# Performance work log

Hardware: AMD Instinct MI355X
Metric: run time of the kernel (lower is better)

Reference implementation:

```python
import jax, jax.numpy as jnp
import numpy as np

B, U, D, N, O = 128, 16, 256, 1024, 256
RES_CONN, IN_CONN, BIAS_P = 0.2, 0.2, 0.5


def _fixed_bernoulli(rng, heads, rows, cols, conn):
    # each column has exactly nb = int(conn*rows) ones (as in the torch code)
    nb = max(1, int(conn * rows))
    r = rng.random((heads, rows, cols))
    thr = np.sort(r, axis=1)[:, nb - 1:nb, :]
    return (r <= thr).astype(np.float32)


def setup_inputs() -> dict:
    rng = np.random.default_rng(0)
    # recurrent weights: normal * fixed-bernoulli mask, normalized by spectral radius
    W = rng.normal(size=(U, N, N)).astype(np.float32) * _fixed_bernoulli(rng, U, N, N, RES_CONN)
    sr0 = np.abs(np.linalg.eigvals(W.astype(np.float64))).max(axis=-1).astype(np.float32).reshape(U, 1, 1)
    W = W / sr0
    Win = _fixed_bernoulli(rng, U, D, N, IN_CONN)
    bias = (rng.random((U, 1, N)) < BIAS_P).astype(np.float32)
    Wout = rng.normal(size=(U, N, O)).astype(np.float32)
    adaptive_lr = rng.random((U, D, 1)).astype(np.float32)
    sr = rng.random((U, 1, 1)).astype(np.float32)
    temperature = np.ones((1,), np.float32)
    X = rng.normal(size=(B, U, D)).astype(np.float32)
    state = rng.normal(size=(B, U, N)).astype(np.float32)
    arrs = dict(X=X, state=state, W=W, Win=Win, bias=bias, Wout=Wout,
                sr=sr, adaptive_lr=adaptive_lr, temperature=temperature)
    return {k: jnp.asarray(v) for k, v in arrs.items()}


def reference(X, state, W, Win, bias, Wout, sr, adaptive_lr, temperature):
    # X: [B,U,D] -> [B,U,1,D]; state: [B,U,N] -> [B,U,1,N]
    x = X[:, :, None, :]
    s = state[:, :, None, :]
    # adaptive per-unit learning rate: softmax over the units axis
    lr = jax.nn.softmax(jnp.einsum('buid,udk->buik', x, adaptive_lr) / temperature, axis=1)  # [B,U,1,1]
    feed = jnp.einsum('buid,udn->buin', x, Win)            # [B,U,1,N]
    echo = jnp.einsum('buin,unm->buim', s, W * sr) + bias  # [B,U,1,N]
    new_state = (1.0 - lr) * s + lr * jnp.tanh(feed + echo)
    output = jnp.einsum('buin,uno->buio', new_state, Wout)  # [B,U,1,O]
    return new_state[:, :, 0, :], output[:, :, 0, :]
```

## Files before the change

kernel.cpp:

```cpp
#include <hip/hip_runtime.h>
#include <math.h>

#define Bsz 128
#define Usz 16
#define Dsz 256
#define Nsz 1024
#define Osz 256

typedef __attribute__((ext_vector_type(4))) float f32x4;
typedef __attribute__((ext_vector_type(8))) short bf16x8;
typedef __attribute__((ext_vector_type(4))) unsigned int u32x4;

union cell_u { u32x4 u; bf16x8 b; };

__device__ __forceinline__ unsigned int fbits(float f) {
    union { float f; unsigned int u; } v; v.f = f; return v.u;
}
__device__ __forceinline__ unsigned int pk(float lo, float hi) {
    return __builtin_amdgcn_perm(fbits(hi), fbits(lo), 0x07060302u);
}
__device__ __forceinline__ bf16x8 pk8s(const float* x, float s) {
    float t[8];
    #pragma unroll
    for (int i = 0; i < 8; i++) t[i] = x[i] * s;
    cell_u r;
    r.u[0] = pk(t[0], t[1]); r.u[1] = pk(t[2], t[3]);
    r.u[2] = pk(t[4], t[5]); r.u[3] = pk(t[6], t[7]);
    return r.b;
}

__global__ __launch_bounds__(256)
void lr_kernel(const float* __restrict__ X, const float* __restrict__ alr,
               const float* __restrict__ temp, float* __restrict__ lr)
{
    const int b = blockIdx.x;
    const int t = threadIdx.x;
    const int u = t >> 4;
    const int l = t & 15;
    const float* xp = X + ((size_t)b * Usz + u) * Dsz;
    const float* ap = alr + (size_t)u * Dsz;
    float s = 0.f;
    for (int d = l; d < Dsz; d += 16) s += xp[d] * ap[d];
    s += __shfl_down(s, 8, 16);
    s += __shfl_down(s, 4, 16);
    s += __shfl_down(s, 2, 16);
    s += __shfl_down(s, 1, 16);
    __shared__ float logits[16];
    if (l == 0) logits[u] = s;
    __syncthreads();
    if (t < 16) {
        const float T = temp[0];
        float m = -1e30f;
        #pragma unroll
        for (int i = 0; i < 16; i++) m = fmaxf(m, logits[i] / T);
        float sum = 0.f;
        #pragma unroll
        for (int i = 0; i < 16; i++) sum += expf(logits[i] / T - m);
        lr[(size_t)b * Usz + t] = expf(logits[t] / T - m) / sum;
    }
}

__global__ __launch_bounds__(256)
void state_mfma(const float* __restrict__ X, const float* __restrict__ state,
                const float* __restrict__ W, const float* __restrict__ Win,
                const float* __restrict__ bias, const float* __restrict__ sr,
                const float* __restrict__ lr, float* __restrict__ out0)
{
    const int id = blockIdx.x;
    const int u  = id & 15;
    const int nt = (id >> 4) & 15;
    const int mt = id >> 8;

    const int tid  = threadIdx.x;
    const int wave = tid >> 6, lane = tid & 63;
    const int l16  = lane & 15, kgl = lane >> 4;
    const int wm = wave & 1, wn = wave >> 1;

    const int row0 = mt * 64 + wm * 32 + l16;
    const int col0 = nt * 64 + wn * 32 + l16;

    const float sru = sr[u];

    const float* Ax0 = X + ((size_t)row0 * Usz + u) * Dsz;
    const float* Ax1 = X + ((size_t)(row0 + 16) * Usz + u) * Dsz;
    const float* Ae0 = state + ((size_t)row0 * Usz + u) * Nsz;
    const float* Ae1 = state + ((size_t)(row0 + 16) * Usz + u) * Nsz;
    const float* Bf  = Win + (size_t)u * Dsz * Nsz + col0;
    const float* Be  = W   + (size_t)u * Nsz * Nsz + col0;

    f32x4 acc[2][2] = {};

    auto loadStep = [&](int step, float (&A0)[8], float (&A1)[8],
                        float (&B0)[8], float (&B1)[8]) {
        const int kb = step * 32 + kgl * 8;
        const float *pa0, *pa1, *pb;
        if (kb < Dsz) {
            pa0 = Ax0 + kb; pa1 = Ax1 + kb; pb = Bf + (size_t)kb * Nsz;
        } else {
            const int kk = kb - Dsz;
            pa0 = Ae0 + kk; pa1 = Ae1 + kk; pb = Be + (size_t)kk * Nsz;
        }
        *(f32x4*)&A0[0] = *(const f32x4*)pa0;
        *(f32x4*)&A0[4] = *(const f32x4*)(pa0 + 4);
        *(f32x4*)&A1[0] = *(const f32x4*)pa1;
        *(f32x4*)&A1[4] = *(const f32x4*)(pa1 + 4);
        #pragma unroll
        for (int j = 0; j < 8; j++) {
            B0[j] = pb[(size_t)j * Nsz];
            B1[j] = pb[(size_t)j * Nsz + 16];
        }
    };
    auto compute = [&](int step, float (&A0)[8], float (&A1)[8],
                       float (&B0)[8], float (&B1)[8]) {
        const float asc = (step < 8) ? 1.f : sru;
        const bf16x8 af0 = pk8s(A0, asc), af1 = pk8s(A1, asc);
        const bf16x8 bf0 = pk8s(B0, 1.f), bf1 = pk8s(B1, 1.f);
        acc[0][0] = __builtin_amdgcn_mfma_f32_16x16x32_bf16(af0, bf0, acc[0][0], 0, 0, 0);
        acc[0][1] = __builtin_amdgcn_mfma_f32_16x16x32_bf16(af0, bf1, acc[0][1], 0, 0, 0);
        acc[1][0] = __builtin_amdgcn_mfma_f32_16x16x32_bf16(af1, bf0, acc[1][0], 0, 0, 0);
        acc[1][1] = __builtin_amdgcn_mfma_f32_16x16x32_bf16(af1, bf1, acc[1][1], 0, 0, 0);
    };

    float A0a[8], A1a[8], B0a[8], B1a[8];
    float A0b[8], A1b[8], B0b[8], B1b[8];

    loadStep(0, A0a, A1a, B0a, B1a);
    for (int s = 0; s < 40; s += 2) {
        loadStep(s + 1, A0b, A1b, B0b, B1b);
        compute(s, A0a, A1a, B0a, B1a);
        if (s + 2 < 40) loadStep(s + 2, A0a, A1a, B0a, B1a);
        compute(s + 1, A0b, A1b, B0b, B1b);
    }

    #pragma unroll
    for (int ni = 0; ni < 2; ni++) {
        const int gcol = nt * 64 + wn * 32 + ni * 16 + l16;
        const float bi = bias[u * Nsz + gcol];
        #pragma unroll
        for (int mi = 0; mi < 2; mi++) {
            #pragma unroll
            for (int rg = 0; rg < 4; rg++) {
                const int grow = mt * 64 + wm * 32 + mi * 16 + kgl * 4 + rg;
                const size_t idx = ((size_t)grow * Usz + u) * Nsz + gcol;
                const float th = tanhf(acc[mi][ni][rg] + bi);
                const float sv = state[idx];
                const float lv = lr[grow * Usz + u];
                out0[idx] = (1.f - lv) * sv + lv * th;
            }
        }
    }
}

__global__ __launch_bounds__(256)
void out_mfma(const float* __restrict__ ns, const float* __restrict__ Wout,
              float* __restrict__ out1)
{
    const int w  = blockIdx.x * 4 + (threadIdx.x >> 6);
    const int u  = w & 15;
    const int ot = (w >> 4) & 15;
    const int mtw = w >> 8;

    const int lane = threadIdx.x & 63;
    const int l16  = lane & 15, kgl = lane >> 4;

    const float* Ap = ns + ((size_t)(mtw * 16 + l16) * Usz + u) * Nsz;
    const float* Bp = Wout + (size_t)u * Nsz * Osz + ot * 16 + l16;

    f32x4 acc = {};

    auto loadStep = [&](int step, float (&A)[8], float (&B)[8]) {
        const int kb = step * 32 + kgl * 8;
        *(f32x4*)&A[0] = *(const f32x4*)(Ap + kb);
        *(f32x4*)&A[4] = *(const f32x4*)(Ap + kb + 4);
        const float* bp = Bp + (size_t)kb * Osz;
        #pragma unroll
        for (int j = 0; j < 8; j++) B[j] = bp[(size_t)j * Osz];
    };
    auto compute = [&](float (&A)[8], float (&B)[8]) {
        const bf16x8 af = pk8s(A, 1.f);
        const bf16x8 bf = pk8s(B, 1.f);
        acc = __builtin_amdgcn_mfma_f32_16x16x32_bf16(af, bf, acc, 0, 0, 0);
    };

    float Aa[8], Ba[8], Ab[8], Bb[8];
    loadStep(0, Aa, Ba);
    for (int s = 0; s < 32; s += 2) {
        loadStep(s + 1, Ab, Bb);
        compute(Aa, Ba);
        if (s + 2 < 32) loadStep(s + 2, Aa, Ba);
        compute(Ab, Bb);
    }

    const int gcol = ot * 16 + l16;
    #pragma unroll
    for (int rg = 0; rg < 4; rg++) {
        const int grow = mtw * 16 + kgl * 4 + rg;
        out1[((size_t)grow * Usz + u) * Osz + gcol] = acc[rg];
    }
}

extern "C" void kernel_launch(void* const* d_in, const int* in_sizes, int n_in,
                              void* d_out, int out_size, void* d_ws, size_t ws_size,
                              hipStream_t stream)
{
    (void)in_sizes; (void)n_in; (void)out_size; (void)ws_size;
    const float* X     = (const float*)d_in[0];
    const float* state = (const float*)d_in[1];
    const float* W     = (const float*)d_in[2];
    const float* Win   = (const float*)d_in[3];
    const float* bias  = (const float*)d_in[4];
    const float* Wout  = (const float*)d_in[5];
    const float* sr    = (const float*)d_in[6];
    const float* alr   = (const float*)d_in[7];
    const float* temp  = (const float*)d_in[8];

    float* out0 = (float*)d_out;
    float* out1 = out0 + (size_t)Bsz * Usz * Nsz;
    float* lr   = (float*)d_ws;

    lr_kernel<<<Bsz, 256, 0, stream>>>(X, alr, temp, lr);
    state_mfma<<<512, 256, 0, stream>>>(X, state, W, Win, bias, sr, lr, out0);
    out_mfma<<<512, 256, 0, stream>>>(out0, Wout, out1);
}
```

Measured before the change: 218.2 us.

## Stage A tiles in LDS with full-batch M tiles and split-K output GEMM

```diff
diff --git a/kernel.cpp b/kernel.cpp
--- a/kernel.cpp
+++ b/kernel.cpp
@@ -6,12 +6,15 @@
 #define Dsz 256
 #define Nsz 1024
 #define Osz 256
-
+#define BK  64
+
+typedef __attribute__((ext_vector_type(2))) unsigned int u32x2;
+typedef __attribute__((ext_vector_type(4))) unsigned int u32x4;
 typedef __attribute__((ext_vector_type(4))) float f32x4;
 typedef __attribute__((ext_vector_type(8))) short bf16x8;
-typedef __attribute__((ext_vector_type(4))) unsigned int u32x4;
 
 union cell_u { u32x4 u; bf16x8 b; };
+union cell2_u { u32x2 u; };
 
 __device__ __forceinline__ unsigned int fbits(float f) {
     union { float f; unsigned int u; } v; v.f = f; return v.u;
@@ -19,13 +22,17 @@
 __device__ __forceinline__ unsigned int pk(float lo, float hi) {
     return __builtin_amdgcn_perm(fbits(hi), fbits(lo), 0x07060302u);
 }
-__device__ __forceinline__ bf16x8 pk8s(const float* x, float s) {
-    float t[8];
-    #pragma unroll
-    for (int i = 0; i < 8; i++) t[i] = x[i] * s;
+__device__ __forceinline__ u32x2 pk4(f32x4 v, float s) {
+    v *= s;
+    u32x2 r; r[0] = pk(v[0], v[1]); r[1] = pk(v[2], v[3]);
+    return r;
+}
+__device__ __forceinline__ bf16x8 ldB8(const float* p, size_t str) {
+    const float x0 = p[0],       x1 = p[str],     x2 = p[2*str], x3 = p[3*str];
+    const float x4 = p[4*str],   x5 = p[5*str],   x6 = p[6*str], x7 = p[7*str];
     cell_u r;
-    r.u[0] = pk(t[0], t[1]); r.u[1] = pk(t[2], t[3]);
-    r.u[2] = pk(t[4], t[5]); r.u[3] = pk(t[6], t[7]);
+    r.u[0] = pk(x0, x1); r.u[1] = pk(x2, x3);
+    r.u[2] = pk(x4, x5); r.u[3] = pk(x6, x7);
     return r.b;
 }
 
@@ -61,75 +68,80 @@
 }
 
 __global__ __launch_bounds__(256)
-void state_mfma(const float* __restrict__ X, const float* __restrict__ state,
+void state_gemm(const float* __restrict__ X, const float* __restrict__ state,
                 const float* __restrict__ W, const float* __restrict__ Win,
                 const float* __restrict__ bias, const float* __restrict__ sr,
                 const float* __restrict__ lr, float* __restrict__ out0)
 {
     const int id = blockIdx.x;
     const int u  = id & 15;
-    const int nt = (id >> 4) & 15;
-    const int mt = id >> 8;
+    const int nt = id >> 4;
 
     const int tid  = threadIdx.x;
     const int wave = tid >> 6, lane = tid & 63;
     const int l16  = lane & 15, kgl = lane >> 4;
     const int wm = wave & 1, wn = wave >> 1;
 
-    const int row0 = mt * 64 + wm * 32 + l16;
-    const int col0 = nt * 64 + wn * 32 + l16;
+    __shared__ unsigned short As[2][128 * 72];
 
     const float sru = sr[u];
 
-    const float* Ax0 = X + ((size_t)row0 * Usz + u) * Dsz;
-    const float* Ax1 = X + ((size_t)(row0 + 16) * Usz + u) * Dsz;
-    const float* Ae0 = state + ((size_t)row0 * Usz + u) * Nsz;
-    const float* Ae1 = state + ((size_t)(row0 + 16) * Usz + u) * Nsz;
-    const float* Bf  = Win + (size_t)u * Dsz * Nsz + col0;
-    const float* Be  = W   + (size_t)u * Nsz * Nsz + col0;
-
-    f32x4 acc[2][2] = {};
-
-    auto loadStep = [&](int step, float (&A0)[8], float (&A1)[8],
-                        float (&B0)[8], float (&B1)[8]) {
-        const int kb = step * 32 + kgl * 8;
-        const float *pa0, *pa1, *pb;
-        if (kb < Dsz) {
-            pa0 = Ax0 + kb; pa1 = Ax1 + kb; pb = Bf + (size_t)kb * Nsz;
+    const int r0 = tid >> 4;
+    const int c  = tid & 15;
+
+    f32x4 ra[8];
+
+    auto ldA = [&](int s) {
+        const int k0 = s * BK;
+        if (k0 < Dsz) {
+            const float* base = X + ((size_t)r0 * Usz + u) * Dsz + k0 + c * 4;
+            #pragma unroll
+            for (int i = 0; i < 8; i++)
+                ra[i] = *(const f32x4*)(base + (size_t)16 * i * Usz * Dsz);
         } else {
-            const int kk = kb - Dsz;
-            pa0 = Ae0 + kk; pa1 = Ae1 + kk; pb = Be + (size_t)kk * Nsz;
-        }
-        *(f32x4*)&A0[0] = *(const f32x4*)pa0;
-        *(f32x4*)&A0[4] = *(const f32x4*)(pa0 + 4);
-        *(f32x4*)&A1[0] = *(const f32x4*)pa1;
-        *(f32x4*)&A1[4] = *(const f32x4*)(pa1 + 4);
-        #pragma unroll
-        for (int j = 0; j < 8; j++) {
-            B0[j] = pb[(size_t)j * Nsz];
-            B1[j] = pb[(size_t)j * Nsz + 16];
-        }
-    };
-    auto compute = [&](int step, float (&A0)[8], float (&A1)[8],
-                       float (&B0)[8], float (&B1)[8]) {
-        const float asc = (step < 8) ? 1.f : sru;
-        const bf16x8 af0 = pk8s(A0, asc), af1 = pk8s(A1, asc);
-        const bf16x8 bf0 = pk8s(B0, 1.f), bf1 = pk8s(B1, 1.f);
-        acc[0][0] = __builtin_amdgcn_mfma_f32_16x16x32_bf16(af0, bf0, acc[0][0], 0, 0, 0);
-        acc[0][1] = __builtin_amdgcn_mfma_f32_16x16x32_bf16(af0, bf1, acc[0][1], 0, 0, 0);
-        acc[1][0] = __builtin_amdgcn_mfma_f32_16x16x32_bf16(af1, bf0, acc[1][0], 0, 0, 0);
-        acc[1][1] = __builtin_amdgcn_mfma_f32_16x16x32_bf16(af1, bf1, acc[1][1], 0, 0, 0);
-    };
-
-    float A0a[8], A1a[8], B0a[8], B1a[8];
-    float A0b[8], A1b[8], B0b[8], B1b[8];
-
-    loadStep(0, A0a, A1a, B0a, B1a);
-    for (int s = 0; s < 40; s += 2) {
-        loadStep(s + 1, A0b, A1b, B0b, B1b);
-        compute(s, A0a, A1a, B0a, B1a);
-        if (s + 2 < 40) loadStep(s + 2, A0a, A1a, B0a, B1a);
-        compute(s + 1, A0b, A1b, B0b, B1b);
+            const float* base = state + ((size_t)r0 * Usz + u) * Nsz + (k0 - Dsz) + c * 4;
+            #pragma unroll
+            for (int i = 0; i < 8; i++)
+                ra[i] = *(const f32x4*)(base + (size_t)16 * i * Usz * Nsz);
+        }
+    };
+    auto wrA = [&](int p, float sc) {
+        #pragma unroll
+        for (int i = 0; i < 8; i++)
+            *(u32x2*)&As[p][(r0 + 16 * i) * 72 + c * 4] = pk4(ra[i], sc);
+    };
+
+    f32x4 acc[4][2] = {};
+
+    auto comp = [&](int s, int p) {
+        const int k0 = s * BK;
+        const float* bbase = (k0 < Dsz)
+            ? Win + (size_t)u * Dsz * Nsz + (size_t)k0 * Nsz
+            : W   + (size_t)u * Nsz * Nsz + (size_t)(k0 - Dsz) * Nsz;
+        const int col = nt * 64 + wn * 32 + l16;
+        #pragma unroll
+        for (int kk = 0; kk < 2; kk++) {
+            const float* bp = bbase + (size_t)(kk * 32 + kgl * 8) * Nsz + col;
+            const bf16x8 bf0 = ldB8(bp, Nsz);
+            const bf16x8 bf1 = ldB8(bp + 16, Nsz);
+            #pragma unroll
+            for (int mi = 0; mi < 4; mi++) {
+                const bf16x8 af = *(const bf16x8*)&As[p][(wm * 64 + mi * 16 + l16) * 72 + kk * 32 + kgl * 8];
+                acc[mi][0] = __builtin_amdgcn_mfma_f32_16x16x32_bf16(af, bf0, acc[mi][0], 0, 0, 0);
+                acc[mi][1] = __builtin_amdgcn_mfma_f32_16x16x32_bf16(af, bf1, acc[mi][1], 0, 0, 0);
+            }
+        }
+    };
+
+    ldA(0); wrA(0, 1.f);
+    ldA(1);
+    __syncthreads();
+    for (int s = 0; s < 20; s++) {
+        const int p = s & 1;
+        if (s + 1 < 20) wrA(p ^ 1, (s + 1 < 4) ? 1.f : sru);
+        if (s + 2 < 20) ldA(s + 2);
+        comp(s, p);
+        __syncthreads();
     }
 
     #pragma unroll
@@ -137,73 +149,121 @@
         const int gcol = nt * 64 + wn * 32 + ni * 16 + l16;
         const float bi = bias[u * Nsz + gcol];
         #pragma unroll
-        for (int mi = 0; mi < 2; mi++) {
+        for (int mi = 0; mi < 4; mi++) {
             #pragma unroll
             for (int rg = 0; rg < 4; rg++) {
-                const int grow = mt * 64 + wm * 32 + mi * 16 + kgl * 4 + rg;
+                const int grow = wm * 64 + mi * 16 + kgl * 4 + rg;
                 const size_t idx = ((size_t)grow * Usz + u) * Nsz + gcol;
                 const float th = tanhf(acc[mi][ni][rg] + bi);
-                const float sv = state[idx];
                 const float lv = lr[grow * Usz + u];
-                out0[idx] = (1.f - lv) * sv + lv * th;
-            }
-        }
-    }
-}
-
-__global__ __launch_bounds__(256)
-void out_mfma(const float* __restrict__ ns, const float* __restrict__ Wout,
-              float* __restrict__ out1)
-{
-    const int w  = blockIdx.x * 4 + (threadIdx.x >> 6);
-    const int u  = w & 15;
-    const int ot = (w >> 4) & 15;
-    const int mtw = w >> 8;
-
-    const int lane = threadIdx.x & 63;
+                out0[idx] = (1.f - lv) * state[idx] + lv * th;
+            }
+        }
+    }
+}
+
+__global__ __launch_bounds__(256)
+void out_gemm(const float* __restrict__ ns, const float* __restrict__ Wout,
+              float* __restrict__ dst, int nsteps, int partial)
+{
+    const int id = blockIdx.x;
+    const int u  = id & 15;
+    const int ot = (id >> 4) & 3;
+    const int ks = id >> 6;
+    const int kbase = ks * nsteps * BK;
+
+    const int tid  = threadIdx.x;
+    const int wave = tid >> 6, lane = tid & 63;
     const int l16  = lane & 15, kgl = lane >> 4;
-
-    const float* Ap = ns + ((size_t)(mtw * 16 + l16) * Usz + u) * Nsz;
-    const float* Bp = Wout + (size_t)u * Nsz * Osz + ot * 16 + l16;
-
-    f32x4 acc = {};
-
-    auto loadStep = [&](int step, float (&A)[8], float (&B)[8]) {
-        const int kb = step * 32 + kgl * 8;
-        *(f32x4*)&A[0] = *(const f32x4*)(Ap + kb);
-        *(f32x4*)&A[4] = *(const f32x4*)(Ap + kb + 4);
-        const float* bp = Bp + (size_t)kb * Osz;
-        #pragma unroll
-        for (int j = 0; j < 8; j++) B[j] = bp[(size_t)j * Osz];
-    };
-    auto compute = [&](float (&A)[8], float (&B)[8]) {
-        const bf16x8 af = pk8s(A, 1.f);
-        const bf16x8 bf = pk8s(B, 1.f);
-        acc = __builtin_amdgcn_mfma_f32_16x16x32_bf16(af, bf, acc, 0, 0, 0);
-    };
-
-    float Aa[8], Ba[8], Ab[8], Bb[8];
-    loadStep(0, Aa, Ba);
-    for (int s = 0; s < 32; s += 2) {
-        loadStep(s + 1, Ab, Bb);
-        compute(Aa, Ba);
-        if (s + 2 < 32) loadStep(s + 2, Aa, Ba);
-        compute(Ab, Bb);
-    }
-
-    const int gcol = ot * 16 + l16;
+    const int wm = wave & 1, wn = wave >> 1;
+
+    __shared__ unsigned short As[2][128 * 72];
+
+    const int r0 = tid >> 4;
+    const int c  = tid & 15;
+
+    f32x4 ra[8];
+    auto ldA = [&](int s) {
+        const float* base = ns + ((size_t)r0 * Usz + u) * Nsz + kbase + s * BK + c * 4;
+        #pragma unroll
+        for (int i = 0; i < 8; i++)
+            ra[i] = *(const f32x4*)(base + (size_t)16 * i * Usz * Nsz);
+    };
+    auto wrA = [&](int p) {
+        #pragma unroll
+        for (int i = 0; i < 8; i++)
+            *(u32x2*)&As[p][(r0 + 16 * i) * 72 + c * 4] = pk4(ra[i], 1.f);
+    };
+
+    f32x4 acc[4][2] = {};
+    auto comp = [&](int s, int p) {
+        const float* bbase = Wout + (size_t)u * Nsz * Osz + (size_t)(kbase + s * BK) * Osz;
+        const int col = ot * 64 + wn * 32 + l16;
+        #pragma unroll
+        for (int kk = 0; kk < 2; kk++) {
+            const float* bp = bbase + (size_t)(kk * 32 + kgl * 8) * Osz + col;
+            const bf16x8 bf0 = ldB8(bp, Osz);
+            const bf16x8 bf1 = ldB8(bp + 16, Osz);
+            #pragma unroll
+            for (int mi = 0; mi < 4; mi++) {
+                const bf16x8 af = *(const bf16x8*)&As[p][(wm * 64 + mi * 16 + l16) * 72 + kk * 32 + kgl * 8];
+                acc[mi][0] = __builtin_amdgcn_mfma_f32_16x16x32_bf16(af, bf0, acc[mi][0], 0, 0, 0);
+                acc[mi][1] = __builtin_amdgcn_mfma_f32_16x16x32_bf16(af, bf1, acc[mi][1], 0, 0, 0);
+            }
+        }
+    };
+
+    ldA(0); wrA(0);
+    if (nsteps > 1) ldA(1);
+    __syncthreads();
+    for (int s = 0; s < nsteps; s++) {
+        const int p = s & 1;
+        if (s + 1 < nsteps) wrA(p ^ 1);
+        if (s + 2 < nsteps) ldA(s + 2);
+        comp(s, p);
+        __syncthreads();
+    }
+
     #pragma unroll
-    for (int rg = 0; rg < 4; rg++) {
-        const int grow = mtw * 16 + kgl * 4 + rg;
-        out1[((size_t)grow * Usz + u) * Osz + gcol] = acc[rg];
-    }
+    for (int ni = 0; ni < 2; ni++) {
+        const int gcol = ot * 64 + wn * 32 + ni * 16 + l16;
+        #pragma unroll
+        for (int mi = 0; mi < 4; mi++) {
+            #pragma unroll
+            for (int rg = 0; rg < 4; rg++) {
+                const int grow = wm * 64 + mi * 16 + kgl * 4 + rg;
+                if (partial)
+                    dst[(((size_t)ks * 16 + u) * 128 + grow) * 256 + gcol] = acc[mi][ni][rg];
+                else
+                    dst[((size_t)grow * Usz + u) * Osz + gcol] = acc[mi][ni][rg];
+            }
+        }
+    }
+}
+
+__global__ __launch_bounds__(256)
+void out_reduce(const float* __restrict__ part, float* __restrict__ out1)
+{
+    const size_t i = (size_t)blockIdx.x * 256 + threadIdx.x;
+    const size_t base = i * 4;
+    const int m = (int)(base >> 12);
+    const int u = (int)((base >> 8) & 15);
+    const int o = (int)(base & 255);
+
+    const size_t pb = ((size_t)u * 128 + m) * 256 + o;
+    const size_t slab = (size_t)16 * 128 * 256;
+    f32x4 s = *(const f32x4*)(part + pb);
+    s += *(const f32x4*)(part + pb + slab);
+    s += *(const f32x4*)(part + pb + 2 * slab);
+    s += *(const f32x4*)(part + pb + 3 * slab);
+    *(f32x4*)(out1 + base) = s;
 }
 
 extern "C" void kernel_launch(void* const* d_in, const int* in_sizes, int n_in,
                               void* d_out, int out_size, void* d_ws, size_t ws_size,
                               hipStream_t stream)
 {
-    (void)in_sizes; (void)n_in; (void)out_size; (void)ws_size;
+    (void)in_sizes; (void)n_in; (void)out_size;
     const float* X     = (const float*)d_in[0];
     const float* state = (const float*)d_in[1];
     const float* W     = (const float*)d_in[2];
@@ -218,7 +278,17 @@
     float* out1 = out0 + (size_t)Bsz * Usz * Nsz;
     float* lr   = (float*)d_ws;
 
+    const size_t p_off   = 8192;
+    const size_t p_bytes = (size_t)4 * 16 * 128 * 256 * 4;
+
     lr_kernel<<<Bsz, 256, 0, stream>>>(X, alr, temp, lr);
-    state_mfma<<<512, 256, 0, stream>>>(X, state, W, Win, bias, sr, lr, out0);
-    out_mfma<<<512, 256, 0, stream>>>(out0, Wout, out1);
-}
+    state_gemm<<<256, 256, 0, stream>>>(X, state, W, Win, bias, sr, lr, out0);
+
+    if (ws_size >= p_off + p_bytes) {
+        float* part = (float*)((char*)d_ws + p_off);
+        out_gemm<<<256, 256, 0, stream>>>(out0, Wout, part, 4, 1);
+        out_reduce<<<512, 256, 0, stream>>>(part, out1);
+    } else {
+        out_gemm<<<64, 256, 0, stream>>>(out0, Wout, out1, 16, 0);
+    }
+}
```

Result: faster. 194.3 us (-11.0%).
